# Kernel tuning notes

Hardware: AMD Instinct MI355X
Metric: run time of the kernel (lower is better)

The kernel has to match this reference:

```python
import jax, jax.numpy as jnp
import numpy as np

DIM = 384
K = 7          # kernel_size
FINAL = 16     # final_size
DROP_P = 0.2


def setup_inputs() -> dict:
    key = jax.random.key(0)
    k1, k2, k3, k4, k5, k6 = jax.random.split(key, 6)
    hr_feats = jax.random.normal(k1, (8, DIM, 112, 112), jnp.float32)
    guidance = jnp.zeros((1,), jnp.float32)  # unused by forward
    dropout_u = jax.random.uniform(k2, (8, FINAL, FINAL, 1), jnp.float32)
    aw = jax.random.normal(k3, (DIM,), jnp.float32) / np.sqrt(DIM).astype(np.float32)
    ab = 0.01 * jax.random.normal(k4, (1,), jnp.float32)
    w = 1.0 + 0.01 * jax.random.normal(k5, (K, K), jnp.float32)
    b = 0.01 * jax.random.normal(k6, (K, K), jnp.float32)
    return {"hr_feats": hr_feats, "guidance": guidance, "dropout_u": dropout_u,
            "aw": aw, "ab": ab, "w": w, "b": b}


def _unfold_patches(x):
    # x: [b, c, h, w] -> [b, nH, nW, K*K, c], matching torch Unfold + reshape/permute
    bs, c, h, wd = x.shape
    stride = (h - K) // (FINAL - 1)
    nH = FINAL
    nW = FINAL * (wd // h)
    r = (jnp.arange(nH) * stride)[:, None] + jnp.arange(K)      # [nH, K]
    cc = (jnp.arange(nW) * stride)[:, None] + jnp.arange(K)     # [nW, K]
    # advanced indexing -> [b, c, nH, nW, K, K]
    patches = x[:, :, r[:, None, :, None], cc[None, :, None, :]]
    # (kh, kw) flattened row-major, channel last -> same ordering as torch Unfold
    return patches.transpose(0, 2, 3, 4, 5, 1).reshape(bs, nH, nW, K * K, c)


def reference(hr_feats, guidance, dropout_u, aw, ab, w, b):
    patches = _unfold_patches(hr_feats)                    # [b, H, W, P, C]
    # attention_net (eval-mode Dropout is identity): Linear(dim, 1)
    logits = jnp.einsum('bhwpc,c->bhwp', patches, aw) + ab[0]
    mask = (dropout_u > DROP_P).astype(logits.dtype)       # [b, H, W, 1]
    attn_logits = logits * mask * w.reshape(1, 1, 1, -1) + b.reshape(1, 1, 1, -1)
    attn = jax.nn.softmax(attn_logits, axis=-1)            # softmax over patches
    return jnp.einsum('bhwpc,bhwp->bchw', patches, attn)   # [b, C, H, W]
```

## Files before the change

### kernel.cpp

```cpp
#include <hip/hip_runtime.h>
#include <cmath>

#define DIM 384
#define IMG 112
#define IMG2 (IMG*IMG)
#define QIMG2 (IMG2/4)
#define FINALN 16
#define PATCH 49
#define DROP_P 0.2f
#define NS 8
#define CPS (DIM/NS)


__global__ __launch_bounds__(256) void kA(const float4* __restrict__ hr4,
                                          const float* __restrict__ aw,
                                          float4* __restrict__ Wp4) {
    __shared__ float s_aw[CPS];
    int tid = threadIdx.x;
    int s = blockIdx.y;
    if (tid < CPS) s_aw[tid] = aw[s * CPS + tid];
    __syncthreads();
    int pid4 = blockIdx.x * 256 + tid;
    int b    = pid4 / QIMG2;
    int rem  = pid4 - b * QIMG2;
    const float4* p = hr4 + (size_t)(b * DIM + s * CPS) * QIMG2 + rem;
    float a0 = 0.f, a1 = 0.f, a2 = 0.f, a3 = 0.f;
    #pragma unroll 12
    for (int c = 0; c < CPS; ++c) {
        float4 v = p[(size_t)c * QIMG2];
        float w = s_aw[c];
        a0 = fmaf(v.x, w, a0);
        a1 = fmaf(v.y, w, a1);
        a2 = fmaf(v.z, w, a2);
        a3 = fmaf(v.w, w, a3);
    }
    Wp4[s * 25088 + pid4] = make_float4(a0, a1, a2, a3);
}

__global__ __launch_bounds__(256) void kB(const float* __restrict__ Wp,
                                          const float* __restrict__ du,
                                          const float* __restrict__ ab,
                                          const float* __restrict__ wmat,
                                          const float* __restrict__ bmat,
                                          float* __restrict__ attn) {
    int tid  = threadIdx.x;
    int lane = tid & 63;
    int t    = blockIdx.x * 4 + (tid >> 6);
    int b = t >> 8;
    int h = (t >> 4) & 15;
    int w = t & 15;
    float mask = (du[t] > DROP_P) ? 1.0f : 0.0f;
    float abv  = ab[0];

    float al = -1e30f;
    float e  = 0.f;
    if (lane < PATCH) {
        int i = lane / 7;
        int j = lane - i * 7;
        int pix = b * IMG2 + (7 * h + i) * IMG + 7 * w + j;
        float logit = abv;
        #pragma unroll
        for (int s = 0; s < NS; ++s) logit += Wp[s * 100352 + pix];
        al = fmaf(logit * mask, wmat[lane], bmat[lane]);
    }
    float m = al;
    #pragma unroll
    for (int d = 32; d >= 1; d >>= 1) m = fmaxf(m, __shfl_xor(m, d, 64));
    e = (lane < PATCH) ? __expf(al - m) : 0.f;
    float ssum = e;
    #pragma unroll
    for (int d = 32; d >= 1; d >>= 1) ssum += __shfl_xor(ssum, d, 64);
    if (lane < PATCH) attn[t * PATCH + lane] = e / ssum;
}

__global__ __launch_bounds__(256) void kC(const float* __restrict__ hr,
                                          const float* __restrict__ attn,
                                          float* __restrict__ out) {
    int blk = blockIdx.x;
    int cg  = blk % 24;
    int h   = (blk / 24) % FINALN;
    int b   = blk / (24 * FINALN);

    __shared__ float s_attn[FINALN * PATCH];
    int tid = threadIdx.x;
    const float* abase = attn + (size_t)(b * 256 + h * 16) * PATCH;
    for (int i = tid; i < FINALN * PATCH; i += 256) s_attn[i] = abase[i];
    __syncthreads();

    int c = cg * 16 + (tid >> 4);
    int w = tid & 15;
    const float* p  = hr + (size_t)(b * DIM + c) * IMG2 + (7 * h) * IMG + 7 * w;
    const float* ap = s_attn + w * PATCH;

    float acc = 0.f;
    #pragma unroll
    for (int i = 0; i < 7; ++i) {
        #pragma unroll
        for (int j = 0; j < 7; ++j) {
            acc = fmaf(p[i * IMG + j], ap[i * 7 + j], acc);
        }
    }
    out[((size_t)(b * DIM + c) * FINALN + h) * FINALN + w] = acc;
}

extern "C" void kernel_launch(void* const* d_in, const int* in_sizes, int n_in,
                              void* d_out, int out_size, void* d_ws, size_t ws_size,
                              hipStream_t stream) {
    const float* hr   = (const float*)d_in[0];
    const float* du   = (const float*)d_in[2];
    const float* aw   = (const float*)d_in[3];
    const float* ab   = (const float*)d_in[4];
    const float* wmat = (const float*)d_in[5];
    const float* bmat = (const float*)d_in[6];
    float* out = (float*)d_out;

    float* Wp   = (float*)d_ws;
    float* attn = Wp + NS * IMG2 * 8;

    kA<<<dim3(98, NS), 256, 0, stream>>>((const float4*)hr, aw, (float4*)Wp);
    kB<<<512, 256, 0, stream>>>(Wp, du, ab, wmat, bmat, attn);
    kC<<<3072, 256, 0, stream>>>(hr, attn, out);
}
```

Before: 255.6 us.

## Fuse logits, softmax and weighted sum into one patch-per-block kernel

Replaces the three-kernel pipeline (channel-split logit partials, softmax, weighted patch sum) with one kernel. Each block stages one 384x49 patch in LDS, reduces the logits, applies the mask and softmax, then computes the attention-weighted sum per channel. Block indices are interleaved across w so neighbouring blocks touch nearby cache lines. This reads hr_feats from HBM once instead of twice and drops the workspace round trip and two launches. The cost is 7-float row gathers that coalesce poorly, and about 75KB of LDS per block, which limits occupancy.

```diff
diff --git a/kernel.cpp b/kernel.cpp
--- a/kernel.cpp
+++ b/kernel.cpp
@@ -4,103 +4,81 @@
 #define DIM 384
 #define IMG 112
 #define IMG2 (IMG*IMG)
-#define QIMG2 (IMG2/4)
 #define FINALN 16
 #define PATCH 49
 #define DROP_P 0.2f
-#define NS 8
-#define CPS (DIM/NS)
 
+__global__ __launch_bounds__(512) void kFused(const float* __restrict__ hr,
+                                              const float* __restrict__ du,
+                                              const float* __restrict__ aw,
+                                              const float* __restrict__ ab,
+                                              const float* __restrict__ wmat,
+                                              const float* __restrict__ bmat,
+                                              float* __restrict__ out) {
+    __shared__ float sp[DIM * PATCH];
+    __shared__ float s_aw[DIM];
+    __shared__ float s_red[256];
 
-__global__ __launch_bounds__(256) void kA(const float4* __restrict__ hr4,
-                                          const float* __restrict__ aw,
-                                          float4* __restrict__ Wp4) {
-    __shared__ float s_aw[CPS];
     int tid = threadIdx.x;
-    int s = blockIdx.y;
-    if (tid < CPS) s_aw[tid] = aw[s * CPS + tid];
-    __syncthreads();
-    int pid4 = blockIdx.x * 256 + tid;
-    int b    = pid4 / QIMG2;
-    int rem  = pid4 - b * QIMG2;
-    const float4* p = hr4 + (size_t)(b * DIM + s * CPS) * QIMG2 + rem;
-    float a0 = 0.f, a1 = 0.f, a2 = 0.f, a3 = 0.f;
-    #pragma unroll 12
-    for (int c = 0; c < CPS; ++c) {
-        float4 v = p[(size_t)c * QIMG2];
-        float w = s_aw[c];
-        a0 = fmaf(v.x, w, a0);
-        a1 = fmaf(v.y, w, a1);
-        a2 = fmaf(v.z, w, a2);
-        a3 = fmaf(v.w, w, a3);
+
+    int id  = blockIdx.x;
+    int nid = (id & 7) * 256 + (id >> 3);
+    int b = nid >> 8;
+    int h = (nid >> 4) & 15;
+    int w = nid & 15;
+
+    for (int i = tid; i < DIM; i += 512) s_aw[i] = aw[i];
+
+    const float* base = hr + (size_t)b * DIM * IMG2 + (size_t)(7 * h) * IMG + 7 * w;
+    for (int r = tid; r < DIM * 7; r += 512) {
+        int c = r / 7;
+        int i = r - c * 7;
+        const float* p = base + (size_t)c * IMG2 + i * IMG;
+        float* d = sp + c * PATCH + i * 7;
+        #pragma unroll
+        for (int j = 0; j < 7; ++j) d[j] = p[j];
     }
-    Wp4[s * 25088 + pid4] = make_float4(a0, a1, a2, a3);
-}
-
-__global__ __launch_bounds__(256) void kB(const float* __restrict__ Wp,
-                                          const float* __restrict__ du,
-                                          const float* __restrict__ ab,
-                                          const float* __restrict__ wmat,
-                                          const float* __restrict__ bmat,
-                                          float* __restrict__ attn) {
-    int tid  = threadIdx.x;
-    int lane = tid & 63;
-    int t    = blockIdx.x * 4 + (tid >> 6);
-    int b = t >> 8;
-    int h = (t >> 4) & 15;
-    int w = t & 15;
-    float mask = (du[t] > DROP_P) ? 1.0f : 0.0f;
-    float abv  = ab[0];
-
-    float al = -1e30f;
-    float e  = 0.f;
-    if (lane < PATCH) {
-        int i = lane / 7;
-        int j = lane - i * 7;
-        int pix = b * IMG2 + (7 * h + i) * IMG + 7 * w + j;
-        float logit = abv;
-        #pragma unroll
-        for (int s = 0; s < NS; ++s) logit += Wp[s * 100352 + pix];
-        al = fmaf(logit * mask, wmat[lane], bmat[lane]);
-    }
-    float m = al;
-    #pragma unroll
-    for (int d = 32; d >= 1; d >>= 1) m = fmaxf(m, __shfl_xor(m, d, 64));
-    e = (lane < PATCH) ? __expf(al - m) : 0.f;
-    float ssum = e;
-    #pragma unroll
-    for (int d = 32; d >= 1; d >>= 1) ssum += __shfl_xor(ssum, d, 64);
-    if (lane < PATCH) attn[t * PATCH + lane] = e / ssum;
-}
-
-__global__ __launch_bounds__(256) void kC(const float* __restrict__ hr,
-                                          const float* __restrict__ attn,
-                                          float* __restrict__ out) {
-    int blk = blockIdx.x;
-    int cg  = blk % 24;
-    int h   = (blk / 24) % FINALN;
-    int b   = blk / (24 * FINALN);
-
-    __shared__ float s_attn[FINALN * PATCH];
-    int tid = threadIdx.x;
-    const float* abase = attn + (size_t)(b * 256 + h * 16) * PATCH;
-    for (int i = tid; i < FINALN * PATCH; i += 256) s_attn[i] = abase[i];
     __syncthreads();
 
-    int c = cg * 16 + (tid >> 4);
-    int w = tid & 15;
-    const float* p  = hr + (size_t)(b * DIM + c) * IMG2 + (7 * h) * IMG + 7 * w;
-    const float* ap = s_attn + w * PATCH;
+    if (tid < 4 * PATCH) {
+        int g = tid / PATCH;
+        int p = tid - g * PATCH;
+        int c0 = g * 96;
+        float acc = 0.f;
+        #pragma unroll 8
+        for (int c = 0; c < 96; ++c)
+            acc = fmaf(sp[(c0 + c) * PATCH + p], s_aw[c0 + c], acc);
+        s_red[tid] = acc;
+    }
+    __syncthreads();
 
-    float acc = 0.f;
-    #pragma unroll
-    for (int i = 0; i < 7; ++i) {
+    if (tid < 64) {
+        float al = -1e30f;
+        if (tid < PATCH) {
+            float logit = s_red[tid] + s_red[PATCH + tid] + s_red[2 * PATCH + tid]
+                        + s_red[3 * PATCH + tid] + ab[0];
+            float mask = (du[(b << 8) + (h << 4) + w] > DROP_P) ? 1.0f : 0.0f;
+            al = fmaf(logit * mask, wmat[tid], bmat[tid]);
+        }
+        float m = al;
         #pragma unroll
-        for (int j = 0; j < 7; ++j) {
-            acc = fmaf(p[i * IMG + j], ap[i * 7 + j], acc);
-        }
+        for (int d = 32; d >= 1; d >>= 1) m = fmaxf(m, __shfl_xor(m, d, 64));
+        float e = (tid < PATCH) ? __expf(al - m) : 0.f;
+        float s = e;
+        #pragma unroll
+        for (int d = 32; d >= 1; d >>= 1) s += __shfl_xor(s, d, 64);
+        if (tid < PATCH) s_red[tid] = e / s;
     }
-    out[((size_t)(b * DIM + c) * FINALN + h) * FINALN + w] = acc;
+    __syncthreads();
+
+    if (tid < DIM) {
+        const float* pc = sp + tid * PATCH;
+        float acc = 0.f;
+        #pragma unroll
+        for (int p = 0; p < PATCH; ++p)
+            acc = fmaf(pc[p], s_red[p], acc);
+        out[(((size_t)b * DIM + tid) * FINALN + h) * FINALN + w] = acc;
+    }
 }
 
 extern "C" void kernel_launch(void* const* d_in, const int* in_sizes, int n_in,
@@ -114,10 +92,5 @@
     const float* bmat = (const float*)d_in[6];
     float* out = (float*)d_out;
 
-    float* Wp   = (float*)d_ws;
-    float* attn = Wp + NS * IMG2 * 8;
-
-    kA<<<dim3(98, NS), 256, 0, stream>>>((const float4*)hr, aw, (float4*)Wp);
-    kB<<<512, 256, 0, stream>>>(Wp, du, ab, wmat, bmat, attn);
-    kC<<<3072, 256, 0, stream>>>(hr, attn, out);
+    kFused<<<2048, 512, 0, stream>>>(hr, du, aw, ab, wmat, bmat, out);
 }
```

Result: no change. 250.7 us (-1.9%).
